# Optimization experiments

Measured on AMD Instinct MI355X. Metric: run time of the kernel, lower is better.

Reference implementation:

```python
import jax, jax.numpy as jnp
import numpy as np

B, S, F, H = 2, 2048, 1024, 16
D = F // H  # 64 head dim


def setup_inputs() -> dict:
    key = jax.random.key(0)
    ks = jax.random.split(key, 11)
    std = 1.0 / np.sqrt(F)
    inp = {
        "q": jax.random.normal(ks[0], (B, S, F), dtype=jnp.float32),
        "k": jax.random.normal(ks[1], (B, S, F), dtype=jnp.float32),
        "v": jax.random.normal(ks[2], (B, S, F), dtype=jnp.float32),
        "wq_w": jax.random.normal(ks[3], (F, F), dtype=jnp.float32) * std,
        "wq_b": jnp.zeros((F,), dtype=jnp.float32),
        "wk_w": jax.random.normal(ks[4], (F, F), dtype=jnp.float32) * std,
        "wk_b": jnp.zeros((F,), dtype=jnp.float32),
        "wv_w": jax.random.normal(ks[5], (F, F), dtype=jnp.float32) * std,
        "wv_b": jnp.zeros((F,), dtype=jnp.float32),
        "fc_w": jax.random.normal(ks[6], (F, F), dtype=jnp.float32) * std,
        "fc_b": jnp.zeros((F,), dtype=jnp.float32),
    }
    return inp


def _split_heads(x):
    # [B, S, F] -> [B, H, S, D]
    return x.reshape(B, S, H, D).transpose(0, 2, 1, 3)


def reference(q, k, v, wq_w, wq_b, wk_w, wk_b, wv_w, wv_b, fc_w, fc_b):
    # Linear projections (torch Linear: x @ W^T + b)
    qh = _split_heads(q @ wq_w.T + wq_b)
    kh = _split_heads(k @ wk_w.T + wk_b)
    vh = _split_heads(v @ wv_w.T + wv_b)
    # scaled dot product attention, explicit [B,H,S,S] scores as in source
    scale = 1.0 / np.sqrt(D)
    scores = jnp.einsum("bhqd,bhkd->bhqk", qh, kh) * scale
    attn = jax.nn.softmax(scores, axis=-1)
    ctx = jnp.einsum("bhqk,bhkd->bhqd", attn, vh)
    # merge heads: [B,H,S,D] -> [B,S,F]
    concat = ctx.transpose(0, 2, 1, 3).reshape(B, S, F)
    out = concat @ fc_w.T + fc_b
    out = jax.nn.relu(out)  # activation=F.relu_ default
    return (out, attn)
```

## Files before the change

### kernel.cpp

```cpp
#include <hip/hip_runtime.h>
#include <stdint.h>

#define DEV __device__ __forceinline__

using f32x4  = __attribute__((ext_vector_type(4))) float;
using bf16x8 = __attribute__((ext_vector_type(8))) __bf16;
using bf16x4 = __attribute__((ext_vector_type(4))) __bf16;

static constexpr int SEQ  = 2048;
static constexpr int FEA  = 1024;
static constexpr int NHEAD = 16;
static constexpr int MROWS = 4096;
static constexpr float QK_SCALE = 0.18033688011112042f;

DEV f32x4 mfma16(bf16x8 a, bf16x8 b, f32x4 c) {
  return __builtin_amdgcn_mfma_f32_16x16x32_bf16(a, b, c, 0, 0, 0);
}

DEV void gload16(const void* g, void* l) {
  __builtin_amdgcn_global_load_lds((__attribute__((address_space(1))) void*)g,
                                   (__attribute__((address_space(3))) void*)l,
                                   16, 0, 0);
}

#define FENCE_VMCNT(n) asm volatile("s_waitcnt vmcnt(" #n ")" ::: "memory")
#define FENCE_LGKM0()  asm volatile("s_waitcnt lgkmcnt(0)" ::: "memory")

struct ConvSeg { const float* src; __bf16* dst; int n4; float scale; };
struct ConvArgs { ConvSeg seg[7]; };

__global__ __launch_bounds__(256) void convert_k(ConvArgs a) {
  const ConvSeg sg = a.seg[blockIdx.y];
  const int stride = gridDim.x * blockDim.x;
  for (int i = blockIdx.x * blockDim.x + threadIdx.x; i < sg.n4; i += stride) {
    const f32x4 v = *(const f32x4*)(sg.src + (size_t)i * 4);
    bf16x4 o = {(__bf16)(v[0] * sg.scale), (__bf16)(v[1] * sg.scale),
                (__bf16)(v[2] * sg.scale), (__bf16)(v[3] * sg.scale)};
    *(bf16x4*)(sg.dst + (size_t)i * 4) = o;
  }
}

DEV void gemm_core64(const __bf16* __restrict__ A, const __bf16* __restrict__ Bt,
                     char* lds, int row0, int col0, int tid, f32x4 (&acc)[4][4]) {
  char* Alds = lds;
  char* Blds = lds + 16384;
  constexpr int K = 1024;
  const int lane = tid & 63;
  const int w    = tid >> 6;
  const int ci   = lane & 15;
  const int g    = lane >> 4;
  const int wr   = w >> 1, wc = w & 1;

  const __bf16* gA[4]; const __bf16* gB[4];
  char* lA[4]; char* lB[4];
#pragma unroll
  for (int j = 0; j < 4; ++j) {
    const int c = tid + 256 * j;
    const int r = c >> 3, s = c & 7;
    const int gsw = (s ^ (r & 7)) * 8;
    gA[j] = A  + (size_t)(row0 + r) * K + gsw;
    gB[j] = Bt + (size_t)(col0 + r) * K + gsw;
    lA[j] = Alds + c * 16;
    lB[j] = Blds + c * 16;
  }
  const int rsw = (ci & 7) << 4;

  for (int k0 = 0; k0 < K; k0 += 64) {
    __syncthreads();
#pragma unroll
    for (int j = 0; j < 4; ++j) {
      gload16(gA[j] + k0, lA[j]);
      gload16(gB[j] + k0, lB[j]);
    }
    __syncthreads();
#pragma unroll
    for (int kk = 0; kk < 2; ++kk) {
      bf16x8 af[4], bfr[4];
#pragma unroll
      for (int m = 0; m < 4; ++m)
        af[m] = *(const bf16x8*)(Alds + (wr * 64 + m * 16 + ci) * 128 +
                                 ((kk * 64 + g * 16) ^ rsw));
#pragma unroll
      for (int n = 0; n < 4; ++n)
        bfr[n] = *(const bf16x8*)(Blds + (wc * 64 + n * 16 + ci) * 128 +
                                  ((kk * 64 + g * 16) ^ rsw));
#pragma unroll
      for (int m = 0; m < 4; ++m)
#pragma unroll
        for (int n = 0; n < 4; ++n)
          acc[m][n] = mfma16(af[m], bfr[n], acc[m][n]);
    }
  }
}

struct QkvArgs {
  const __bf16* A[3];
  const __bf16* Bt[3];
  const float*  bias[3];
  float         bscale[3];
  __bf16*       out[3];
};

__global__ __launch_bounds__(256) void gemm_qkv(QkvArgs args) {
  __shared__ __align__(16) char lds[32768];
  const int z = blockIdx.z;
  const int tid = threadIdx.x;
  const int row0 = blockIdx.x * 128;
  const int col0 = blockIdx.y * 128;
  f32x4 acc[4][4] = {};
  gemm_core64(args.A[z], args.Bt[z], lds, row0, col0, tid, acc);

  const int lane = tid & 63;
  const int ci = lane & 15, g = lane >> 4;
  const int w = tid >> 6;
  const int wr = w >> 1, wc = w & 1;
  const float* bias = args.bias[z];
  const float bscale = args.bscale[z];
  __bf16* outp = args.out[z];
  const bool vt = (z == 2);
#pragma unroll
  for (int m = 0; m < 4; ++m)
#pragma unroll
    for (int n = 0; n < 4; ++n)
#pragma unroll
      for (int r = 0; r < 4; ++r) {
        const int gr = row0 + wr * 64 + m * 16 + 4 * g + r;
        const int gc = col0 + wc * 64 + n * 16 + ci;
        const float vv = acc[m][n][r] + bias[gc] * bscale;
        const int b = gr >> 11, s = gr & (SEQ - 1);
        const int h = gc >> 6,  d = gc & 63;
        if (!vt)
          outp[(((size_t)b * NHEAD + h) * SEQ + s) * 64 + d] = (__bf16)vv;
        else
          outp[(((size_t)b * NHEAD + h) * 64 + d) * SEQ + s] = (__bf16)vv;
      }
}

__global__ __launch_bounds__(256) void gemm_fc(const __bf16* __restrict__ A,
                                               const __bf16* __restrict__ Bt,
                                               const float* __restrict__ bias,
                                               float* __restrict__ outp) {
  __shared__ __align__(16) char lds[32768];
  const int tid = threadIdx.x;
  const int row0 = blockIdx.x * 128;
  const int col0 = blockIdx.y * 128;
  f32x4 acc[4][4] = {};
  gemm_core64(A, Bt, lds, row0, col0, tid, acc);

  const int lane = tid & 63;
  const int ci = lane & 15, g = lane >> 4;
  const int w = tid >> 6;
  const int wr = w >> 1, wc = w & 1;
#pragma unroll
  for (int m = 0; m < 4; ++m)
#pragma unroll
    for (int n = 0; n < 4; ++n)
#pragma unroll
      for (int r = 0; r < 4; ++r) {
        const int gr = row0 + wr * 64 + m * 16 + 4 * g + r;
        const int gc = col0 + wc * 64 + n * 16 + ci;
        const float vv = fmaxf(acc[m][n][r] + bias[gc], 0.0f);
        __builtin_nontemporal_store(vv, &outp[(size_t)gr * FEA + gc]);
      }
}

static constexpr int QBLK = 32;
static constexpr int GQT  = 4;
static constexpr int KVB  = 128;
static constexpr int NT   = SEQ / KVB;

__global__ __launch_bounds__(512, 4) void attn_fused(const __bf16* __restrict__ Qh,
                                                     const __bf16* __restrict__ Kh,
                                                     const __bf16* __restrict__ VhT,
                                                     float* __restrict__ attn_out,
                                                     __bf16* __restrict__ Cbuf) {
  __shared__ __align__(16) char smem[65536];
  __shared__ float rs_lds[8][16];
  __shared__ float linv_lds[QBLK];
  float* pvf = (float*)smem;

  const int tid  = threadIdx.x;
  const int lane = tid & 63;
  const int w    = tid >> 6;
  const int ci   = lane & 15;
  const int g    = lane >> 4;
  const int qg   = w >> 2;
  const int kg   = w & 3;

  const int id   = blockIdx.x;
  const int xcd  = id & 7;
  const int idx  = id >> 3;
  const int bh   = xcd * 4 + (idx >> 4);
  const int qgrp = idx & 15;

  const __bf16* Qbase = Qh + ((size_t)bh * SEQ + (size_t)qgrp * (QBLK * GQT)) * 64;
  const char*   Kbyt  = (const char*)(Kh  + (size_t)bh * SEQ * 64);
  const char*   Vbyt  = (const char*)(VhT + (size_t)bh * 64 * SEQ);

  const int cA = tid, cB = tid + 512;
  const int kgoffA = ((cA >> 3) * 128) + (((cA & 7) ^ ((cA >> 3) & 7)) * 16);
  const int kgoffB = ((cB >> 3) * 128) + (((cB & 7) ^ ((cB >> 3) & 7)) * 16);
  const int vdA = cA >> 4, vdB = cB >> 4;
  const int vgoffA = vdA * (SEQ * 2) + (((cA & 15) ^ (vdA & 7)) * 16);
  const int vgoffB = vdB * (SEQ * 2) + (((cB & 15) ^ (vdB & 7)) * 16);

#define STAGE_K(t, boff) { gload16(Kbyt + (size_t)(t) * 16384 + kgoffA, smem + (boff) + cA * 16); \
                           gload16(Kbyt + (size_t)(t) * 16384 + kgoffB, smem + (boff) + cB * 16); }
#define STAGE_V(t, boff) { gload16(Vbyt + (size_t)(t) * 256 + vgoffA, smem + 16384 + (boff) + cA * 16); \
                           gload16(Vbyt + (size_t)(t) * 256 + vgoffB, smem + 16384 + (boff) + cB * 16); }

  const int kswz  = (ci & 7) << 4;
  const int krow0 = kg * 4096 + ci * 128;

  bf16x8 cq0, cq1;
  {
    const __bf16* qp = Qbase + (qg * 16 + ci) * 64;
    cq0 = *(const bf16x8*)(qp + 8 * g);
    cq1 = *(const bf16x8*)(qp + 32 + 8 * g);
  }

  float rs = 0.f;
  STAGE_K(0, 0);
  STAGE_K(1, 16384);
  for (int p = 0; p < NT / 2; ++p) {
    const int base = (p & 1) << 15;
    __builtin_amdgcn_s_barrier();
    if (p < NT / 2 - 1) {
      STAGE_K(2 * p + 2, base ^ 32768);
      STAGE_K(2 * p + 3, (base ^ 32768) + 16384);
      FENCE_VMCNT(4);
    } else {
      FENCE_VMCNT(0);
    }
    __builtin_amdgcn_s_setprio(1);
#pragma unroll
    for (int hb = 0; hb < 2; ++hb) {
      const char* kt = smem + base + hb * 16384 + krow0;
#pragma unroll
      for (int s = 0; s < 2; ++s) {
        const bf16x8 k0 = *(const bf16x8*)(kt + s * 2048 + ((16 * g) ^ kswz));
        const bf16x8 k1 = *(const bf16x8*)(kt + s * 2048 + ((64 + 16 * g) ^ kswz));
        f32x4 sf = {0.f, 0.f, 0.f, 0.f};
        sf = mfma16(k0, cq0, sf);
        sf = mfma16(k1, cq1, sf);
#pragma unroll
        for (int r = 0; r < 4; ++r) rs += __builtin_amdgcn_exp2f(sf[r]);
      }
    }
    __builtin_amdgcn_s_setprio(0);
    FENCE_LGKM0();
  }
  rs += __shfl_xor(rs, 16);
  rs += __shfl_xor(rs, 32);
  if (lane < 16) rs_lds[w][lane] = rs;
  __syncthreads();
  if (tid < QBLK) {
    const int qg2 = tid >> 4;
    float ts = 0.f;
#pragma unroll
    for (int kk = 0; kk < 4; ++kk) ts += rs_lds[qg2 * 4 + kk][tid & 15];
    linv_lds[tid] = -__log2f(ts);
  }
  __syncthreads();

  for (int i = 0; i < GQT; ++i) {
    const bool more = (i + 1 < GQT);
    bf16x8 nq0 = {}, nq1 = {};
    if (more) {
      const __bf16* qp = Qbase + ((i + 1) * QBLK + qg * 16 + ci) * 64;
      nq0 = *(const bf16x8*)(qp + 8 * g);
      nq1 = *(const bf16x8*)(qp + 32 + 8 * g);
    }
    const float linv = linv_lds[qg * 16 + ci];
    float* orow = attn_out + ((size_t)bh * SEQ + (size_t)(qgrp * GQT + i) * QBLK +
                              qg * 16 + ci) * SEQ + kg * 32 + 4 * g;
    f32x4 apv[4] = {};
    float nrs = 0.f;

    STAGE_K(0, 0);
    STAGE_V(0, 0);
    for (int t = 0; t < NT; ++t) {
      const int coff = (t & 1) << 15;
      __builtin_amdgcn_s_barrier();
      if (t < NT - 1) {
        STAGE_K(t + 1, coff ^ 32768);
        STAGE_V(t + 1, coff ^ 32768);
        if (t == 0) FENCE_VMCNT(4);
        else        FENCE_VMCNT(6);
      } else {
        FENCE_VMCNT(2);
      }

      __builtin_amdgcn_s_setprio(1);
      f32x4 e[2];
#pragma unroll
      for (int s = 0; s < 2; ++s) {
        const char* kt = smem + coff + krow0 + s * 2048;
        const bf16x8 k0 = *(const bf16x8*)(kt + ((16 * g) ^ kswz));
        const bf16x8 k1 = *(const bf16x8*)(kt + ((64 + 16 * g) ^ kswz));
        f32x4 sf = {0.f, 0.f, 0.f, 0.f};
        sf = mfma16(k0, cq0, sf);
        sf = mfma16(k1, cq1, sf);
        if (more) {
          f32x4 nsf = {0.f, 0.f, 0.f, 0.f};
          nsf = mfma16(k0, nq0, nsf);
          nsf = mfma16(k1, nq1, nsf);
#pragma unroll
          for (int r = 0; r < 4; ++r) nrs += __builtin_amdgcn_exp2f(nsf[r]);
        }
#pragma unroll
        for (int r = 0; r < 4; ++r) e[s][r] = __builtin_amdgcn_exp2f(sf[r] + linv);
      }
      __builtin_nontemporal_store(e[0], (f32x4*)(orow + t * 128));
      __builtin_nontemporal_store(e[1], (f32x4*)(orow + t * 128 + 16));

      const bf16x8 pa = {(__bf16)e[0][0], (__bf16)e[0][1], (__bf16)e[0][2], (__bf16)e[0][3],
                         (__bf16)e[1][0], (__bf16)e[1][1], (__bf16)e[1][2], (__bf16)e[1][3]};
      const int inr0 = (64 * kg + 8 * g) ^ kswz;
      const int inr1 = (64 * kg + 32 + 8 * g) ^ kswz;
#pragma unroll
      for (int dt = 0; dt < 4; ++dt) {
        const char* vrow = smem + 16384 + coff + (dt * 16 + ci) * 256;
        const bf16x4 v0 = *(const bf16x4*)(vrow + inr0);
        const bf16x4 v1 = *(const bf16x4*)(vrow + inr1);
        const bf16x8 vb = {v0[0], v0[1], v0[2], v0[3], v1[0], v1[1], v1[2], v1[3]};
        apv[dt] = mfma16(pa, vb, apv[dt]);
      }
      __builtin_amdgcn_s_setprio(0);
      FENCE_LGKM0();
    }

    __syncthreads();
    {
      const int basew = (qg * 4 + kg) * 16;
#pragma unroll
      for (int dt = 0; dt < 4; ++dt)
#pragma unroll
        for (int r = 0; r < 4; ++r)
          pvf[(basew + 4 * g + r) * 68 + dt * 16 + ci] = apv[dt][r];
    }
    if (more) {
      nrs += __shfl_xor(nrs, 16);
      nrs += __shfl_xor(nrs, 32);
      if (lane < 16) rs_lds[w][lane] = nrs;
    }
    __syncthreads();
    {
      const int qq  = tid >> 4;
      const int d0  = (tid & 15) * 4;
      const int qg2 = qq >> 4, row = qq & 15;
      f32x4 ss = {0.f, 0.f, 0.f, 0.f};
#pragma unroll
      for (int kk = 0; kk < 4; ++kk)
        ss += *(const f32x4*)&pvf[((qg2 * 4 + kk) * 16 + row) * 68 + d0];
      const int b = bh >> 4, h = bh & 15;
      const int srow = (qgrp * GQT + i) * QBLK + qq;
      const bf16x4 o = {(__bf16)ss[0], (__bf16)ss[1], (__bf16)ss[2], (__bf16)ss[3]};
      *(bf16x4*)&Cbuf[((size_t)b * SEQ + srow) * FEA + h * 64 + d0] = o;
    }
    if (more && tid < QBLK) {
      const int qg2 = tid >> 4;
      float ts = 0.f;
#pragma unroll
      for (int kk = 0; kk < 4; ++kk) ts += rs_lds[qg2 * 4 + kk][tid & 15];
      linv_lds[tid] = -__log2f(ts);
    }
    cq0 = nq0; cq1 = nq1;
    FENCE_LGKM0();
    __syncthreads();
  }
#undef STAGE_K
#undef STAGE_V
}

extern "C" void kernel_launch(void* const* d_in, const int* in_sizes, int n_in,
                              void* d_out, int out_size, void* d_ws, size_t ws_size,
                              hipStream_t stream) {
  const float* q    = (const float*)d_in[0];
  const float* k    = (const float*)d_in[1];
  const float* v    = (const float*)d_in[2];
  const float* wq_w = (const float*)d_in[3];
  const float* wq_b = (const float*)d_in[4];
  const float* wk_w = (const float*)d_in[5];
  const float* wk_b = (const float*)d_in[6];
  const float* wv_w = (const float*)d_in[7];
  const float* wv_b = (const float*)d_in[8];
  const float* fc_w = (const float*)d_in[9];
  const float* fc_b = (const float*)d_in[10];

  float* out0 = (float*)d_out;
  float* attn = out0 + (size_t)MROWS * FEA;

  __bf16* Xq = (__bf16*)attn;
  __bf16* Xk = Xq + (size_t)MROWS * FEA;
  __bf16* Xv = Xk + (size_t)MROWS * FEA;
  __bf16* Wq = Xv + (size_t)MROWS * FEA;
  __bf16* Wk = Wq + (size_t)FEA * FEA;
  __bf16* Wv = Wk + (size_t)FEA * FEA;

  __bf16* Qh  = (__bf16*)d_ws;
  __bf16* Kh  = Qh  + (size_t)MROWS * FEA;
  __bf16* VhT = Kh  + (size_t)MROWS * FEA;
  __bf16* Cb  = VhT + (size_t)MROWS * FEA;
  __bf16* Wfc = Cb  + (size_t)MROWS * FEA;

  ConvArgs ca;
  ca.seg[0] = {q,    Xq,  (MROWS * FEA) / 4, 1.0f};
  ca.seg[1] = {k,    Xk,  (MROWS * FEA) / 4, 1.0f};
  ca.seg[2] = {v,    Xv,  (MROWS * FEA) / 4, 1.0f};
  ca.seg[3] = {wq_w, Wq,  (FEA * FEA) / 4,   QK_SCALE};
  ca.seg[4] = {wk_w, Wk,  (FEA * FEA) / 4,   1.0f};
  ca.seg[5] = {wv_w, Wv,  (FEA * FEA) / 4,   1.0f};
  ca.seg[6] = {fc_w, Wfc, (FEA * FEA) / 4,   1.0f};
  convert_k<<<dim3(512, 7), 256, 0, stream>>>(ca);

  QkvArgs qa;
  qa.A[0] = Xq; qa.Bt[0] = Wq; qa.bias[0] = wq_b; qa.bscale[0] = QK_SCALE; qa.out[0] = Qh;
  qa.A[1] = Xk; qa.Bt[1] = Wk; qa.bias[1] = wk_b; qa.bscale[1] = 1.0f;     qa.out[1] = Kh;
  qa.A[2] = Xv; qa.Bt[2] = Wv; qa.bias[2] = wv_b; qa.bscale[2] = 1.0f;     qa.out[2] = VhT;
  gemm_qkv<<<dim3(MROWS / 128, FEA / 128, 3), 256, 0, stream>>>(qa);

  attn_fused<<<dim3(512), 512, 0, stream>>>(Qh, Kh, VhT, attn, Cb);

  gemm_fc<<<dim3(MROWS / 128, FEA / 128), 256, 0, stream>>>(Cb, Wfc, fc_b, out0);
}
```

Measured before the change: 217.9 us.

## Double attention workgroup to 1024 threads with 64-query tiles sharing K/V stages

The fused attention block now uses 1024 threads (16 waves) and processes 64 query rows per tile in 2 iterations instead of 32 rows in 4. Each K/V tile staged into LDS is therefore reused by twice as many query rows, and each thread issues one async load per stage instead of two. The row-sum pass now steps one K tile at a time. The PV reduction through LDS is split into two serialized halves with extra barriers. Larger workgroups raise register pressure and barrier cost, and the launch bound of 8 may be unattainable.

Result: slower. 254.5 us, median of 2 (+16.8%).

```diff
diff --git a/kernel.cpp b/kernel.cpp
--- a/kernel.cpp
+++ b/kernel.cpp
@@ -164,18 +164,18 @@
       }
 }
 
-static constexpr int QBLK = 32;
-static constexpr int GQT  = 4;
+static constexpr int QBLK = 64;
+static constexpr int GQT  = 2;
 static constexpr int KVB  = 128;
 static constexpr int NT   = SEQ / KVB;
 
-__global__ __launch_bounds__(512, 4) void attn_fused(const __bf16* __restrict__ Qh,
-                                                     const __bf16* __restrict__ Kh,
-                                                     const __bf16* __restrict__ VhT,
-                                                     float* __restrict__ attn_out,
-                                                     __bf16* __restrict__ Cbuf) {
+__global__ __launch_bounds__(1024, 8) void attn_fused(const __bf16* __restrict__ Qh,
+                                                      const __bf16* __restrict__ Kh,
+                                                      const __bf16* __restrict__ VhT,
+                                                      float* __restrict__ attn_out,
+                                                      __bf16* __restrict__ Cbuf) {
   __shared__ __align__(16) char smem[65536];
-  __shared__ float rs_lds[8][16];
+  __shared__ float rs_lds[16][16];
   __shared__ float linv_lds[QBLK];
   float* pvf = (float*)smem;
 
@@ -197,17 +197,13 @@
   const char*   Kbyt  = (const char*)(Kh  + (size_t)bh * SEQ * 64);
   const char*   Vbyt  = (const char*)(VhT + (size_t)bh * 64 * SEQ);
 
-  const int cA = tid, cB = tid + 512;
-  const int kgoffA = ((cA >> 3) * 128) + (((cA & 7) ^ ((cA >> 3) & 7)) * 16);
-  const int kgoffB = ((cB >> 3) * 128) + (((cB & 7) ^ ((cB >> 3) & 7)) * 16);
-  const int vdA = cA >> 4, vdB = cB >> 4;
-  const int vgoffA = vdA * (SEQ * 2) + (((cA & 15) ^ (vdA & 7)) * 16);
-  const int vgoffB = vdB * (SEQ * 2) + (((cB & 15) ^ (vdB & 7)) * 16);
-
-#define STAGE_K(t, boff) { gload16(Kbyt + (size_t)(t) * 16384 + kgoffA, smem + (boff) + cA * 16); \
-                           gload16(Kbyt + (size_t)(t) * 16384 + kgoffB, smem + (boff) + cB * 16); }
-#define STAGE_V(t, boff) { gload16(Vbyt + (size_t)(t) * 256 + vgoffA, smem + 16384 + (boff) + cA * 16); \
-                           gload16(Vbyt + (size_t)(t) * 256 + vgoffB, smem + 16384 + (boff) + cB * 16); }
+  const int c  = tid;
+  const int kgoff = ((c >> 3) * 128) + (((c & 7) ^ ((c >> 3) & 7)) * 16);
+  const int vd = c >> 4;
+  const int vgoff = vd * (SEQ * 2) + (((c & 15) ^ (vd & 7)) * 16);
+
+#define STAGE_K(t, boff) gload16(Kbyt + (size_t)(t) * 16384 + kgoff, smem + (boff) + c * 16)
+#define STAGE_V(t, boff) gload16(Vbyt + (size_t)(t) * 256 + vgoff, smem + 16384 + (boff) + c * 16)
 
   const int kswz  = (ci & 7) << 4;
   const int krow0 = kg * 4096 + ci * 128;
@@ -221,31 +217,22 @@
 
   float rs = 0.f;
   STAGE_K(0, 0);
-  STAGE_K(1, 16384);
-  for (int p = 0; p < NT / 2; ++p) {
-    const int base = (p & 1) << 15;
+  for (int t = 0; t < NT; ++t) {
+    const int coff = (t & 1) << 15;
     __builtin_amdgcn_s_barrier();
-    if (p < NT / 2 - 1) {
-      STAGE_K(2 * p + 2, base ^ 32768);
-      STAGE_K(2 * p + 3, (base ^ 32768) + 16384);
-      FENCE_VMCNT(4);
-    } else {
-      FENCE_VMCNT(0);
-    }
+    if (t < NT - 1) { STAGE_K(t + 1, coff ^ 32768); FENCE_VMCNT(1); }
+    else            { FENCE_VMCNT(0); }
     __builtin_amdgcn_s_setprio(1);
-#pragma unroll
-    for (int hb = 0; hb < 2; ++hb) {
-      const char* kt = smem + base + hb * 16384 + krow0;
-#pragma unroll
-      for (int s = 0; s < 2; ++s) {
-        const bf16x8 k0 = *(const bf16x8*)(kt + s * 2048 + ((16 * g) ^ kswz));
-        const bf16x8 k1 = *(const bf16x8*)(kt + s * 2048 + ((64 + 16 * g) ^ kswz));
-        f32x4 sf = {0.f, 0.f, 0.f, 0.f};
-        sf = mfma16(k0, cq0, sf);
-        sf = mfma16(k1, cq1, sf);
-#pragma unroll
-        for (int r = 0; r < 4; ++r) rs += __builtin_amdgcn_exp2f(sf[r]);
-      }
+    const char* kt = smem + coff + krow0;
+#pragma unroll
+    for (int s = 0; s < 2; ++s) {
+      const bf16x8 k0 = *(const bf16x8*)(kt + s * 2048 + ((16 * g) ^ kswz));
+      const bf16x8 k1 = *(const bf16x8*)(kt + s * 2048 + ((64 + 16 * g) ^ kswz));
+      f32x4 sf = {0.f, 0.f, 0.f, 0.f};
+      sf = mfma16(k0, cq0, sf);
+      sf = mfma16(k1, cq1, sf);
+#pragma unroll
+      for (int r = 0; r < 4; ++r) rs += __builtin_amdgcn_exp2f(sf[r]);
     }
     __builtin_amdgcn_s_setprio(0);
     FENCE_LGKM0();
@@ -285,8 +272,8 @@
       if (t < NT - 1) {
         STAGE_K(t + 1, coff ^ 32768);
         STAGE_V(t + 1, coff ^ 32768);
-        if (t == 0) FENCE_VMCNT(4);
-        else        FENCE_VMCNT(6);
+        if (t == 0) FENCE_VMCNT(2);
+        else        FENCE_VMCNT(4);
       } else {
         FENCE_VMCNT(2);
       }
@@ -331,7 +318,7 @@
     }
 
     __syncthreads();
-    {
+    if (qg < 2) {
       const int basew = (qg * 4 + kg) * 16;
 #pragma unroll
       for (int dt = 0; dt < 4; ++dt)
@@ -345,7 +332,8 @@
       if (lane < 16) rs_lds[w][lane] = nrs;
     }
     __syncthreads();
-    {
+    const int b = bh >> 4, h = bh & 15;
+    if (tid < 512) {
       const int qq  = tid >> 4;
       const int d0  = (tid & 15) * 4;
       const int qg2 = qq >> 4, row = qq & 15;
@@ -353,7 +341,6 @@
 #pragma unroll
       for (int kk = 0; kk < 4; ++kk)
         ss += *(const f32x4*)&pvf[((qg2 * 4 + kk) * 16 + row) * 68 + d0];
-      const int b = bh >> 4, h = bh & 15;
       const int srow = (qgrp * GQT + i) * QBLK + qq;
       const bf16x4 o = {(__bf16)ss[0], (__bf16)ss[1], (__bf16)ss[2], (__bf16)ss[3]};
       *(bf16x4*)&Cbuf[((size_t)b * SEQ + srow) * FEA + h * 64 + d0] = o;
@@ -364,6 +351,28 @@
 #pragma unroll
       for (int kk = 0; kk < 4; ++kk) ts += rs_lds[qg2 * 4 + kk][tid & 15];
       linv_lds[tid] = -__log2f(ts);
+    }
+    __syncthreads();
+    if (qg >= 2) {
+      const int basew = ((qg - 2) * 4 + kg) * 16;
+#pragma unroll
+      for (int dt = 0; dt < 4; ++dt)
+#pragma unroll
+        for (int r = 0; r < 4; ++r)
+          pvf[(basew + 4 * g + r) * 68 + dt * 16 + ci] = apv[dt][r];
+    }
+    __syncthreads();
+    if (tid < 512) {
+      const int qq  = tid >> 4;
+      const int d0  = (tid & 15) * 4;
+      const int qg2 = qq >> 4, row = qq & 15;
+      f32x4 ss = {0.f, 0.f, 0.f, 0.f};
+#pragma unroll
+      for (int kk = 0; kk < 4; ++kk)
+        ss += *(const f32x4*)&pvf[((qg2 * 4 + kk) * 16 + row) * 68 + d0];
+      const int srow = (qgrp * GQT + i) * QBLK + 32 + qq;
+      const bf16x4 o = {(__bf16)ss[0], (__bf16)ss[1], (__bf16)ss[2], (__bf16)ss[3]};
+      *(bf16x4*)&Cbuf[((size_t)b * SEQ + srow) * FEA + h * 64 + d0] = o;
     }
     cq0 = nq0; cq1 = nq1;
     FENCE_LGKM0();
@@ -420,7 +429,7 @@
   qa.A[2] = Xv; qa.Bt[2] = Wv; qa.bias[2] = wv_b; qa.bscale[2] = 1.0f;     qa.out[2] = VhT;
   gemm_qkv<<<dim3(MROWS / 128, FEA / 128, 3), 256, 0, stream>>>(qa);
 
-  attn_fused<<<dim3(512), 512, 0, stream>>>(Qh, Kh, VhT, attn, Cb);
+  attn_fused<<<dim3(512), 1024, 0, stream>>>(Qh, Kh, VhT, attn, Cb);
 
   gemm_fc<<<dim3(MROWS / 128, FEA / 128), 256, 0, stream>>>(Cb, Wfc, fc_b, out0);
 }
```
